# Kernel tuning notes

Measured on AMD Instinct MI355X. Metric: run time of the kernel, lower is better.

Reference implementation:

```python
import jax, jax.numpy as jnp
import numpy as np

B, H, W, DIM = 1, 256, 256, 192
HEADS = 6
K, DIL = 7, 2            # NAttention kernel / dilation
WS, DF = 8, 2            # stripe window size, anchor down factor
AWS = WS // DF           # anchor window size (4)
N1, N2 = WS * WS, AWS * AWS
L = H * W
CPB_HID = 512


def _nbr(size, k, d):
    # 1D neighborhood-attention neighbor indices with dilation (edge-clamped)
    i = np.arange(size); g = i % d; p = i // d
    gsize = size // d  # d divides size
    start = np.clip(p - k // 2, 0, gsize - k)
    nbr_p = start[:, None] + np.arange(k)[None, :]
    nbr = g[:, None] + d * nbr_p                    # absolute key index
    rb = nbr_p - p[:, None] + (k - 1)               # rpb index in [0, 2k-2]
    return nbr.astype(np.int32), rb.astype(np.int32)

NBR_H, RB_H = _nbr(H, K, DIL)
NBR_W, RB_W = _nbr(W, K, DIL)


def _na_attention(q, k, v, rpb):
    # q,k,v: (B, heads, H, W, hd); rpb: (heads, 2K-1, 2K-1)
    bias = rpb[:, RB_H, :]                          # (heads,H,K,2K-1)
    bias = jnp.take(bias, RB_W, axis=3)             # (heads,H,K,W,K)
    bias = jnp.transpose(bias, (0, 1, 3, 2, 4))     # (heads,H,W,K,K)
    logits = []
    for ki in range(K):
        kh = jnp.take(k, NBR_H[:, ki], axis=2)
        for kj in range(K):
            khw = jnp.take(kh, NBR_W[:, kj], axis=3)
            logits.append(jnp.einsum('bnhwc,bnhwc->bnhw', q, khw))
    a = jnp.stack(logits, axis=-1).reshape(*q.shape[:4], K, K) + bias[None]
    a = jax.nn.softmax(a.reshape(*q.shape[:4], K * K), axis=-1).reshape(*q.shape[:4], K, K)
    out = jnp.zeros_like(q)
    for ki in range(K):
        vh = jnp.take(v, NBR_H[:, ki], axis=2)
        for kj in range(K):
            vhw = jnp.take(vh, NBR_W[:, kj], axis=3)
            out = out + a[..., ki, kj, None] * vhw
    return out

na_attention = jax.checkpoint(_na_attention)


def window_partition(x, ws):
    b, h, w, c = x.shape
    x = x.reshape(b, h // ws, ws, w // ws, ws, c)
    return jnp.transpose(x, (0, 1, 3, 2, 4, 5)).reshape(-1, ws * ws, c)


def window_reverse(x, ws, h, w):
    c = x.shape[-1]
    b = x.shape[0] // ((h // ws) * (w // ws))
    x = x.reshape(b, h // ws, w // ws, ws, ws, c)
    return jnp.transpose(x, (0, 1, 3, 2, 4, 5)).reshape(b, h, w, c)


def _l2n(x):
    n = jnp.linalg.norm(x, axis=-1, keepdims=True)
    return x / jnp.maximum(n, 1e-12)


def _affine(attn, table, index, ls, w1, b1, w2):
    # attn: (Bw, heads, Na, Nb)
    attn = attn * jnp.exp(jnp.minimum(ls, float(np.log(100.0))))[None]
    bt = jax.nn.relu(table.reshape(-1, 2) @ w1 + b1) @ w2           # (T, heads)
    bias = bt[index.reshape(-1)].reshape(index.shape[0], index.shape[1], HEADS)
    bias = 16.0 * jax.nn.sigmoid(jnp.transpose(bias, (2, 0, 1)))    # (heads,Na,Nb)
    return attn + bias[None]


def _cos_attn(q, k, v, table, index, ls, w1, b1, w2):
    attn = jnp.einsum('bhnc,bhmc->bhnm', _l2n(q), _l2n(k))
    attn = jax.nn.softmax(_affine(attn, table, index, ls, w1, b1, w2), axis=-1)
    return attn @ v


def _forward(x, h_size, w_size, table, index_a2w, index_w2a, qkv_w, qkv_b,
             anchor_dw_w, anchor_dw_b, anchor_pw_w, anchor_pw_b,
             na_qkv_w, na_qkv_b, na_after_w, na_after_b, na_rpb,
             ls1, cpb1_w1, cpb1_b1, cpb1_w2, ls2, cpb2_w1, cpb2_b1, cpb2_w2,
             proj_w, proj_b):
    Bx, Lx, C = x.shape
    Hs, Ws_ = int(h_size), int(w_size)
    qkv = x @ qkv_w + qkv_b                     # (B,L,3C)
    half = C * 3 // 2
    qkv_window, qkv_stripe = qkv[..., :half], qkv[..., half:]
    # anchor projection: depthwise conv (k=DF+1, stride=DF) + pointwise
    xi = x.reshape(Bx, Hs, Ws_, C)
    a = jax.lax.conv_general_dilated(
        xi, anchor_dw_w, (DF, DF), ((1, 1), (1, 1)),
        dimension_numbers=('NHWC', 'HWIO', 'NHWC'), feature_group_count=C) + anchor_dw_b
    a = a @ anchor_pw_w + anchor_pw_b           # (B, H/DF, W/DF, C//2)
    # ---- neighborhood attention branch ----
    hd = C // HEADS
    xw = qkv_window.reshape(Bx, Hs, Ws_, half)
    q2 = (xw @ na_qkv_w + na_qkv_b).reshape(Bx, Hs, Ws_, 3, HEADS, hd)
    q2 = jnp.transpose(q2, (3, 0, 4, 1, 2, 5))  # (3,B,heads,H,W,hd)
    qn, kn, vn = q2[0] * hd ** -0.5, q2[1], q2[2]
    xna = na_attention(qn, kn, vn, na_rpb)
    xna = jnp.transpose(xna, (0, 2, 3, 1, 4)).reshape(Bx, Hs, Ws_, C)
    xna = (xna @ na_after_w + na_after_b).reshape(Bx, Lx, C // 2)
    # ---- anchor stripe attention branch ----
    qs = window_partition(qkv_stripe.reshape(Bx, Hs, Ws_, half), WS)  # (Bw,N1,1.5C)
    an = window_partition(a, AWS)                                     # (Bw,N2,C//2)
    Bw = qs.shape[0]
    hs = C // 2 // HEADS
    q3 = jnp.transpose(qs.reshape(Bw, N1, 3, HEADS, hs), (2, 0, 3, 1, 4))
    q_s, k_s, v_s = q3[0], q3[1], q3[2]
    an = jnp.transpose(an.reshape(Bw, N2, HEADS, hs), (0, 2, 1, 3))
    x1 = _cos_attn(an, k_s, v_s, table, index_a2w, ls1, cpb1_w1, cpb1_b1, cpb1_w2)
    x2 = _cos_attn(q_s, an, x1, table, index_w2a, ls2, cpb2_w1, cpb2_b1, cpb2_w2)
    x2 = jnp.transpose(x2, (0, 2, 1, 3)).reshape(Bw, N1, C // 2)
    xs = window_reverse(x2, WS, Hs, Ws_).reshape(Bx, Lx, C // 2)
    return jnp.concatenate([xna, xs], axis=-1) @ proj_w + proj_b


def setup_inputs() -> dict:
    key = jax.random.key(0)
    ks = jax.random.split(key, 16)
    f = lambda i, shp, s=0.02: jax.random.normal(ks[i], shp, dtype=jnp.float32) * s
    x = jax.random.normal(ks[0], (B, L, DIM), dtype=jnp.float32)
    # swin-v2 style normalized log-spaced relative coords table
    rc = np.arange(-(WS - 1), WS, dtype=np.float32) / (WS - 1)
    t = np.stack(np.meshgrid(rc, rc, indexing='ij'), axis=-1)[None]
    table = jnp.asarray(np.sign(t) * np.log2(1 + np.abs(t) * 8) / 3.0, dtype=jnp.float32)
    wc = np.arange(WS); ac = np.arange(AWS) * DF
    cw = np.stack(np.meshgrid(wc, wc, indexing='ij'), -1).reshape(-1, 2)
    ca = np.stack(np.meshgrid(ac, ac, indexing='ij'), -1).reshape(-1, 2)
    def _idx(c1, c2):
        d = c1[:, None, :] - c2[None, :, :]
        return jnp.asarray((d[..., 0] + WS - 1) * (2 * WS - 1) + (d[..., 1] + WS - 1), dtype=jnp.int32)
    return {
        'x': x, 'h_size': H, 'w_size': W, 'table': table,
        'index_a2w': _idx(ca, cw), 'index_w2a': _idx(cw, ca),
        'qkv_w': f(1, (DIM, 3 * DIM)), 'qkv_b': jnp.zeros((3 * DIM,), jnp.float32),
        'anchor_dw_w': f(2, (DF + 1, DF + 1, 1, DIM), 0.1),
        'anchor_dw_b': jnp.zeros((DIM,), jnp.float32),
        'anchor_pw_w': f(3, (DIM, DIM // 2)), 'anchor_pw_b': jnp.zeros((DIM // 2,), jnp.float32),
        'na_qkv_w': f(4, (3 * DIM // 2, 3 * DIM)), 'na_qkv_b': jnp.zeros((3 * DIM,), jnp.float32),
        'na_after_w': f(5, (DIM, DIM // 2)), 'na_after_b': jnp.zeros((DIM // 2,), jnp.float32),
        'na_rpb': f(6, (HEADS, 2 * K - 1, 2 * K - 1)),
        'ls1': jnp.log(10.0) * jnp.ones((HEADS, 1, 1), jnp.float32),
        'cpb1_w1': f(7, (2, CPB_HID), 0.1), 'cpb1_b1': jnp.zeros((CPB_HID,), jnp.float32),
        'cpb1_w2': f(8, (CPB_HID, HEADS), 0.1),
        'ls2': jnp.log(10.0) * jnp.ones((HEADS, 1, 1), jnp.float32),
        'cpb2_w1': f(9, (2, CPB_HID), 0.1), 'cpb2_b1': jnp.zeros((CPB_HID,), jnp.float32),
        'cpb2_w2': f(10, (CPB_HID, HEADS), 0.1),
        'proj_w': f(11, (DIM, DIM)), 'proj_b': jnp.zeros((DIM,), jnp.float32),
    }


def reference(x, h_size, w_size, table, index_a2w, index_w2a, qkv_w, qkv_b,
              anchor_dw_w, anchor_dw_b, anchor_pw_w, anchor_pw_b,
              na_qkv_w, na_qkv_b, na_after_w, na_after_b, na_rpb,
              ls1, cpb1_w1, cpb1_b1, cpb1_w2, ls2, cpb2_w1, cpb2_b1, cpb2_w2,
              proj_w, proj_b):
    return _forward(x, h_size, w_size, table, index_a2w, index_w2a, qkv_w, qkv_b,
                    anchor_dw_w, anchor_dw_b, anchor_pw_w, anchor_pw_b,
                    na_qkv_w, na_qkv_b, na_after_w, na_after_b, na_rpb,
                    ls1, cpb1_w1, cpb1_b1, cpb1_w2, ls2, cpb2_w1, cpb2_b1, cpb2_w2,
                    proj_w, proj_b)
```

## Files before the change

kernel.cpp:

```cpp
#include <hip/hip_runtime.h>
#include <math.h>


typedef unsigned short bf16_t;
typedef __attribute__((ext_vector_type(8))) short short8;
typedef __attribute__((ext_vector_type(4))) float f32x4;

__device__ inline float bf2f(bf16_t v) { return __uint_as_float((unsigned)v << 16); }
__device__ inline bf16_t f2bf(float f) {
    unsigned u = __float_as_uint(f);
    unsigned r = (u + 0x7fffu + ((u >> 16) & 1u)) >> 16;
    return (bf16_t)r;
}
__device__ inline float cvt(float v) { return v; }
__device__ inline float cvt(bf16_t v) { return bf2f(v); }
__device__ inline void sto(float* p, float v) { *p = v; }
__device__ inline void sto(bf16_t* p, float v) { *p = f2bf(v); }

__device__ inline void ld_bf8(const bf16_t* p, float* d) {
    uint4 r = *(const uint4*)p;
    d[0] = __uint_as_float(r.x << 16); d[1] = __uint_as_float(r.x & 0xffff0000u);
    d[2] = __uint_as_float(r.y << 16); d[3] = __uint_as_float(r.y & 0xffff0000u);
    d[4] = __uint_as_float(r.z << 16); d[5] = __uint_as_float(r.z & 0xffff0000u);
    d[6] = __uint_as_float(r.w << 16); d[7] = __uint_as_float(r.w & 0xffff0000u);
}
__device__ inline unsigned pk2(float a, float b) {
    return (unsigned)f2bf(a) | ((unsigned)f2bf(b) << 16);
}

template <int KD, int NA, typename TO>
__global__ __launch_bounds__(256) void mfma_gemm_k(
    const bf16_t* __restrict__ A, const bf16_t* __restrict__ Bt,
    const float* __restrict__ bias, TO* __restrict__ C,
    int lda, int ldb, int ldc)
{
    const int t = threadIdx.x;
    const int lane = t & 63, wave = t >> 6;
    const int wr = wave >> 1, wc = wave & 1;
    const int m0 = blockIdx.y * 128 + wr * 64;
    const int n0 = blockIdx.x * 96 + wc * 48;
    const int lm = lane & 15;
    const int q  = lane >> 4;

    f32x4 acc[4][3] = {};
    const bf16_t* ap = A + (size_t)(m0 + lm) * lda + q * 8;
    const bf16_t* bp = Bt + (size_t)(n0 + lm) * ldb + q * 8;

#pragma unroll
    for (int k0 = 0; k0 < KD; k0 += 32) {
        short8 af[4], bf[3];
#pragma unroll
        for (int mi = 0; mi < 4; mi++)
            af[mi] = *(const short8*)(ap + (size_t)(mi * 16) * lda + k0);
#pragma unroll
        for (int ni = 0; ni < 3; ni++)
            bf[ni] = *(const short8*)(bp + (size_t)(ni * 16) * ldb + k0);
#pragma unroll
        for (int mi = 0; mi < 4; mi++)
#pragma unroll
            for (int ni = 0; ni < 3; ni++)
                acc[mi][ni] = __builtin_amdgcn_mfma_f32_16x16x32_bf16(
                    af[mi], bf[ni], acc[mi][ni], 0, 0, 0);
    }

#pragma unroll
    for (int mi = 0; mi < 4; mi++) {
#pragma unroll
        for (int ni = 0; ni < 3; ni++) {
            int col = n0 + ni * 16 + lm;
            float bv = bias[col];
            if (NA) {
                int which = col / 192;
                int hh = (col % 192) / 32;
                int d  = col % 32;
                size_t pbase = ((size_t)which * 6 + hh) * ((size_t)65536 * 32) + d;
#pragma unroll
                for (int r = 0; r < 4; r++) {
                    int row = m0 + mi * 16 + q * 4 + r;
                    int ii = row >> 8, jj = row & 255;
                    int par = ((ii & 1) << 1) | (jj & 1);
                    int pix = par * 16384 + (ii >> 1) * 128 + (jj >> 1);
                    sto(&C[pbase + (size_t)pix * 32], acc[mi][ni][r] + bv);
                }
            } else {
#pragma unroll
                for (int r = 0; r < 4; r++) {
                    int row = m0 + mi * 16 + q * 4 + r;
                    sto(&C[(size_t)row * ldc + col], acc[mi][ni][r] + bv);
                }
            }
        }
    }
}

__global__ __launch_bounds__(256) void cvt_bf16_k(
    const float* __restrict__ src, bf16_t* __restrict__ dst, int n8)
{
    int tid = blockIdx.x * 256 + threadIdx.x;
    if (tid >= n8) return;
    float4 a = ((const float4*)src)[tid * 2];
    float4 b = ((const float4*)src)[tid * 2 + 1];
    uint4 o;
    o.x = pk2(a.x, a.y); o.y = pk2(a.z, a.w);
    o.z = pk2(b.x, b.y); o.w = pk2(b.z, b.w);
    ((uint4*)dst)[tid] = o;
}

__global__ __launch_bounds__(256) void tcvt_k(
    const float* __restrict__ W, bf16_t* __restrict__ Wt,
    int Kd, int N, int ld, int coloff)
{
    int tid = blockIdx.x * 256 + threadIdx.x;
    if (tid >= Kd * N) return;
    int k = tid % Kd, n = tid / Kd;
    Wt[tid] = f2bf(W[(size_t)k * ld + coloff + n]);
}

__global__ __launch_bounds__(256) void tpose_qkvw_k(
    const float* __restrict__ W, float* __restrict__ WT)
{
    int tid = blockIdx.x * 256 + threadIdx.x;
    if (tid >= 288 * 192) return;
    int k = tid % 192, j = tid / 192;
    WT[tid] = W[(size_t)k * 576 + j];
}

__global__ __launch_bounds__(256) void fold_wna_t_k(
    const float* __restrict__ qkv_wT, const float* __restrict__ na_qkv_w,
    bf16_t* __restrict__ Wna_t)
{
    int tid = blockIdx.x * 256 + threadIdx.x;
    if (tid >= 576 * 192) return;
    int k = tid % 192, n = tid / 192;
    float acc = 0.f;
    for (int j = 0; j < 288; j++)
        acc += qkv_wT[j * 192 + k] * na_qkv_w[j * 576 + n];
    Wna_t[tid] = f2bf(acc);
}

__global__ __launch_bounds__(256) void fold_bna_k(
    const float* __restrict__ qkv_b, const float* __restrict__ na_qkv_w,
    const float* __restrict__ na_qkv_b, float* __restrict__ bna)
{
    int j = blockIdx.x * 256 + threadIdx.x;
    if (j >= 576) return;
    float acc = na_qkv_b[j];
    for (int k = 0; k < 288; k++)
        acc += qkv_b[k] * na_qkv_w[k * 576 + j];
    bna[j] = acc;
}

__global__ __launch_bounds__(256) void cpb_k(
    const float* __restrict__ table, const float* __restrict__ w1,
    const float* __restrict__ b1, const float* __restrict__ w2,
    float* __restrict__ bt)
{
    int tid = blockIdx.x * 256 + threadIdx.x;
    if (tid >= 225 * 6) return;
    int h = tid % 6, t = tid / 6;
    float t0 = table[t * 2], t1 = table[t * 2 + 1];
    float acc = 0.f;
    for (int m = 0; m < 512; m++) {
        float hv = t0 * w1[m] + t1 * w1[512 + m] + b1[m];
        hv = fmaxf(hv, 0.f);
        acc += hv * w2[m * 6 + h];
    }
    bt[tid] = acc;
}

#define BM 64
#define BN 64
#define BKK 16
template <typename TA, typename TO>
__global__ __launch_bounds__(256) void gemm_k(
    const TA* __restrict__ A, const float* __restrict__ B,
    const float* __restrict__ bias, TO* __restrict__ C,
    int M, int N, int Kd, int lda, int ldb, int ldc)
{
    __shared__ float As[BKK][BM + 1];
    __shared__ float Bs[BKK][BN + 1];
    const int t  = threadIdx.x;
    const int tx = t & 15, ty = t >> 4;
    const int m0 = blockIdx.y * BM, n0 = blockIdx.x * BN;
    float acc[4][4] = {};

    for (int k0 = 0; k0 < Kd; k0 += BKK) {
#pragma unroll
        for (int i = 0; i < 4; i++) {
            int m = (t >> 4) + i * 16;
            int k = t & 15;
            int gm = m0 + m, gk = k0 + k;
            As[k][m] = (gm < M && gk < Kd) ? cvt(A[(size_t)gm * lda + gk]) : 0.f;
        }
#pragma unroll
        for (int i = 0; i < 4; i++) {
            int k = (t >> 6) + i * 4;
            int n = t & 63;
            int gk = k0 + k, gn = n0 + n;
            Bs[k][n] = (gk < Kd && gn < N) ? B[(size_t)gk * ldb + gn] : 0.f;
        }
        __syncthreads();
#pragma unroll
        for (int k = 0; k < BKK; k++) {
            float a[4], b[4];
#pragma unroll
            for (int i = 0; i < 4; i++) a[i] = As[k][ty * 4 + i];
#pragma unroll
            for (int j = 0; j < 4; j++) b[j] = Bs[k][tx * 4 + j];
#pragma unroll
            for (int i = 0; i < 4; i++)
#pragma unroll
                for (int j = 0; j < 4; j++) acc[i][j] += a[i] * b[j];
        }
        __syncthreads();
    }
#pragma unroll
    for (int i = 0; i < 4; i++) {
        int gm = m0 + ty * 4 + i;
        if (gm >= M) continue;
#pragma unroll
        for (int j = 0; j < 4; j++) {
            int gn = n0 + tx * 4 + j;
            if (gn >= N) continue;
            sto(&C[(size_t)gm * ldc + gn], acc[i][j] + bias[gn]);
        }
    }
}

__global__ __launch_bounds__(256) void dwconv_k(
    const float* __restrict__ x, const float* __restrict__ w,
    const float* __restrict__ b, float* __restrict__ adw)
{
    int tid = blockIdx.x * 256 + threadIdx.x;
    if (tid >= 16384 * 48) return;
    int c4 = tid % 48;
    int p = tid / 48;
    int ow = p & 127, oh = p >> 7;
    int c = c4 * 4;
    float4 s = *(const float4*)(b + c);
#pragma unroll
    for (int kh = 0; kh < 3; kh++) {
        int ih = oh * 2 - 1 + kh;
        if (ih < 0 || ih >= 256) continue;
#pragma unroll
        for (int kw = 0; kw < 3; kw++) {
            int iw = ow * 2 - 1 + kw;
            if (iw < 0 || iw >= 256) continue;
            float4 xv = *(const float4*)(x + (size_t)(ih * 256 + iw) * 192 + c);
            float4 wv = *(const float4*)(w + (kh * 3 + kw) * 192 + c);
            s.x += xv.x * wv.x; s.y += xv.y * wv.y;
            s.z += xv.z * wv.z; s.w += xv.w * wv.w;
        }
    }
    *(float4*)(adw + (size_t)p * 192 + c) = s;
}

__global__ __launch_bounds__(256) void na_attn_k(
    const bf16_t* __restrict__ nap, const float* __restrict__ rpb,
    bf16_t* __restrict__ outp)
{
    __shared__ float rpb_s[176];
    __shared__ __align__(16) unsigned P_s[4][16][20];

    const int t = threadIdx.x;
    const int wv = t >> 6, lane = t & 63;
    const int lm = lane & 15, lq = lane >> 4;
    const int z = blockIdx.z;
    const int h = z >> 2, par = z & 3;

    if (t < 169) rpb_s[t] = rpb[h * 169 + t];
    __syncthreads();

    const int pi  = blockIdx.y;
    const int pj0 = blockIdx.x * 64 + wv * 16;
    const int si  = min(max(pi - 3, 0), 121);
    const int rbh0 = si - pi + 6;
    const int c0  = min(max(pj0 - 3, 0), 121) & ~7;

    const size_t plane = (size_t)65536 * 32;
    const size_t poff  = (size_t)(par * 16384) * 32;
    const bf16_t* qpl = nap + (size_t)h * plane + poff;
    const bf16_t* kpl = nap + (size_t)(6 + h) * plane + poff;
    const bf16_t* vpl = nap + (size_t)(12 + h) * plane + poff;

    const short8 qf = *(const short8*)(qpl + ((size_t)(pi * 128 + pj0 + lm)) * 32 + lq * 8);

    int offc[4][2]; bool vm[4][2];
#pragma unroll
    for (int r = 0; r < 4; r++) {
        int q = lq * 4 + r, pj = pj0 + q;
        int sj = min(max(pj - 3, 0), 121);
#pragma unroll
        for (int t2 = 0; t2 < 2; t2++) {
            int c = c0 + 2 * lm + t2;
            vm[r][t2] = (c >= sj) && (c <= sj + 6);
            offc[r][t2] = min(max(c - pj + 6, 0), 12);
        }
    }
    const int kc0 = min(c0 + 2 * lm,     127) * 64;
    const int kc1 = min(c0 + 2 * lm + 1, 127) * 64;
    int vcoff[8];
#pragma unroll
    for (int i = 0; i < 8; i++) vcoff[i] = min(c0 + lq * 8 + i, 127) * 64;

    const float scale = 0.17677669529663687f;
    f32x4 o0 = {}, o1 = {};
    float sums[4] = {0.f, 0.f, 0.f, 0.f};
    const f32x4 zz = {};

#pragma unroll 2
    for (int rr = 0; rr < 7; rr++) {
        const size_t rb2 = (size_t)((si + rr) * 128) * 64;
        const char* krow = (const char*)kpl + rb2;
        const char* vrow = (const char*)vpl + rb2;

        short8 kf0 = *(const short8*)(krow + kc0 + lq * 16);
        short8 kf1 = *(const short8*)(krow + kc1 + lq * 16);
        f32x4 s0 = __builtin_amdgcn_mfma_f32_16x16x32_bf16(qf, kf0, zz, 0, 0, 0);
        f32x4 s1 = __builtin_amdgcn_mfma_f32_16x16x32_bf16(qf, kf1, zz, 0, 0, 0);

        const float* br = rpb_s + (rbh0 + rr) * 13;
        float e0[4], e1[4];
#pragma unroll
        for (int r = 0; r < 4; r++) {
            float a0 = __expf(fmaf(s0[r], scale, br[offc[r][0]]));
            float a1 = __expf(fmaf(s1[r], scale, br[offc[r][1]]));
            a0 = vm[r][0] ? a0 : 0.f;
            a1 = vm[r][1] ? a1 : 0.f;
            e0[r] = a0; e1[r] = a1;
            sums[r] += a0 + a1;
        }
#pragma unroll
        for (int r = 0; r < 4; r++) {
            unsigned pr;
            asm("v_cvt_pk_bf16_f32 %0, %1, %2" : "=v"(pr) : "v"(e0[r]), "v"(e1[r]));
            P_s[wv][lq * 4 + r][lm] = pr;
        }
        const short8 pf = *(const short8*)((const bf16_t*)P_s[wv][lm] + lq * 8);

        short8 vf0, vf1;
        const char* v0b = vrow + lm * 2;
        const char* v1b = vrow + 32 + lm * 2;
#pragma unroll
        for (int i = 0; i < 8; i++) {
            ((bf16_t*)&vf0)[i] = *(const bf16_t*)(v0b + vcoff[i]);
            ((bf16_t*)&vf1)[i] = *(const bf16_t*)(v1b + vcoff[i]);
        }
        o0 = __builtin_amdgcn_mfma_f32_16x16x32_bf16(pf, vf0, o0, 0, 0, 0);
        o1 = __builtin_amdgcn_mfma_f32_16x16x32_bf16(pf, vf1, o1, 0, 0, 0);
    }

#pragma unroll
    for (int r = 0; r < 4; r++) {
        float s = sums[r];
        s += __shfl_xor(s, 1, 64);
        s += __shfl_xor(s, 2, 64);
        s += __shfl_xor(s, 4, 64);
        s += __shfl_xor(s, 8, 64);
        sums[r] = 1.0f / s;
    }

    const int gi = par >> 1, gj = par & 1;
    const int i0 = pi * 2 + gi;
    bf16_t* ob = outp + ((size_t)i0 * 256 + gj) * 192 + h * 32 + lm;
#pragma unroll
    for (int r = 0; r < 4; r++) {
        int q = lq * 4 + r;
        size_t px = (size_t)(pj0 + q) * 2 * 192;
        ob[px]      = f2bf(o0[r] * sums[r]);
        ob[px + 16] = f2bf(o1[r] * sums[r]);
    }
}

__global__ __launch_bounds__(256) void attn1_k(
    const float* __restrict__ apw,
    const bf16_t* __restrict__ qkvs,
    const float* __restrict__ bt1, const int* __restrict__ idx,
    const float* __restrict__ ls1,
    float* __restrict__ x1)
{
    int tid = blockIdx.x * 256 + threadIdx.x;
    if (tid >= 1024 * 6 * 16) return;
    int n2 = tid & 15;
    int h = (tid >> 4) % 6;
    int w = tid / 96;
    int wi = w >> 5, wj = w & 31;
    float scale = __expf(fminf(ls1[h], 4.605170185988091f));

    int ay = wi * 4 + (n2 >> 2), ax = wj * 4 + (n2 & 3);
    const float* ap = apw + (size_t)(ay * 128 + ax) * 96 + h * 16;
    float qv[16]; float nrm = 0.f;
#pragma unroll
    for (int d = 0; d < 16; d += 4) {
        float4 v = *(const float4*)(ap + d);
        qv[d] = v.x; qv[d + 1] = v.y; qv[d + 2] = v.z; qv[d + 3] = v.w;
        nrm += v.x * v.x + v.y * v.y + v.z * v.z + v.w * v.w;
    }
    float innorm = 1.0f / fmaxf(sqrtf(nrm), 1e-12f);
#pragma unroll
    for (int d = 0; d < 16; d++) qv[d] *= innorm;

    float sum = 0.f;
    float acc[16] = {};
#pragma unroll 4
    for (int m = 0; m < 64; m++) {
        int ky = wi * 8 + (m >> 3), kx = wj * 8 + (m & 7);
        const bf16_t* kp = qkvs + (size_t)(ky * 256 + kx) * 288 + 96 + h * 16;
        float kv[16];
        ld_bf8(kp, kv); ld_bf8(kp + 8, kv + 8);
        float dot = 0.f, kn = 0.f;
#pragma unroll
        for (int d = 0; d < 16; d++) { dot += qv[d] * kv[d]; kn += kv[d] * kv[d]; }
        dot *= 1.0f / fmaxf(sqrtf(kn), 1e-12f);
        float bias = 16.0f / (1.0f + __expf(-bt1[idx[n2 * 64 + m] * 6 + h]));
        float e = __expf(dot * scale + bias);
        sum += e;
        const bf16_t* vp = qkvs + (size_t)(ky * 256 + kx) * 288 + 192 + h * 16;
        float vv[16];
        ld_bf8(vp, vv); ld_bf8(vp + 8, vv + 8);
#pragma unroll
        for (int d = 0; d < 16; d++) acc[d] += e * vv[d];
    }
    float inv = 1.0f / sum;
    float* xp = x1 + ((size_t)w * 6 + h) * 256 + n2 * 16;
#pragma unroll
    for (int d = 0; d < 16; d += 4)
        *(float4*)(xp + d) = make_float4(acc[d] * inv, acc[d + 1] * inv,
                                         acc[d + 2] * inv, acc[d + 3] * inv);
}

__global__ __launch_bounds__(256) void attn2_k(
    const float* __restrict__ apw,
    const bf16_t* __restrict__ qkvs,
    const float* __restrict__ bt2, const int* __restrict__ idx,
    const float* __restrict__ ls2,
    const float* __restrict__ x1,
    bf16_t* __restrict__ cat)
{
    int tid = blockIdx.x * 256 + threadIdx.x;
    if (tid >= 1024 * 6 * 64) return;
    int n1 = tid & 63;
    int h = (tid >> 6) % 6;
    int w = tid / 384;
    int wi = w >> 5, wj = w & 31;
    float scale = __expf(fminf(ls2[h], 4.605170185988091f));

    int qy = wi * 8 + (n1 >> 3), qx = wj * 8 + (n1 & 7);
    const bf16_t* qp = qkvs + (size_t)(qy * 256 + qx) * 288 + h * 16;
    float qv[16];
    ld_bf8(qp, qv); ld_bf8(qp + 8, qv + 8);
    float nrm = 0.f;
#pragma unroll
    for (int d = 0; d < 16; d++) nrm += qv[d] * qv[d];
    float innorm = 1.0f / fmaxf(sqrtf(nrm), 1e-12f);
#pragma unroll
    for (int d = 0; d < 16; d++) qv[d] *= innorm;

    float sum = 0.f;
    float acc[16] = {};
#pragma unroll
    for (int m = 0; m < 16; m++) {
        int ay = wi * 4 + (m >> 2), ax = wj * 4 + (m & 3);
        const float* ap = apw + (size_t)(ay * 128 + ax) * 96 + h * 16;
        float dot = 0.f, kn = 0.f;
#pragma unroll
        for (int d = 0; d < 16; d += 4) {
            float4 v = *(const float4*)(ap + d);
            dot += qv[d] * v.x + qv[d + 1] * v.y + qv[d + 2] * v.z + qv[d + 3] * v.w;
            kn += v.x * v.x + v.y * v.y + v.z * v.z + v.w * v.w;
        }
        dot *= 1.0f / fmaxf(sqrtf(kn), 1e-12f);
        float bias = 16.0f / (1.0f + __expf(-bt2[idx[n1 * 16 + m] * 6 + h]));
        float e = __expf(dot * scale + bias);
        sum += e;
        const float* vp = x1 + ((size_t)w * 6 + h) * 256 + m * 16;
#pragma unroll
        for (int d = 0; d < 16; d += 4) {
            float4 v = *(const float4*)(vp + d);
            acc[d] += e * v.x; acc[d + 1] += e * v.y;
            acc[d + 2] += e * v.z; acc[d + 3] += e * v.w;
        }
    }
    float inv = 1.0f / sum;
#pragma unroll
    for (int d = 0; d < 16; d++) acc[d] *= inv;
    bf16_t* op = cat + (size_t)(qy * 256 + qx) * 192 + 96 + h * 16;
    uint4 o0, o1;
    o0.x = pk2(acc[0], acc[1]);   o0.y = pk2(acc[2], acc[3]);
    o0.z = pk2(acc[4], acc[5]);   o0.w = pk2(acc[6], acc[7]);
    o1.x = pk2(acc[8], acc[9]);   o1.y = pk2(acc[10], acc[11]);
    o1.z = pk2(acc[12], acc[13]); o1.w = pk2(acc[14], acc[15]);
    *(uint4*)(op) = o0;
    *(uint4*)(op + 8) = o1;
}

extern "C" void kernel_launch(void* const* d_in, const int* in_sizes, int n_in,
                              void* d_out, int out_size, void* d_ws, size_t ws_size,
                              hipStream_t stream) {
    const float* x          = (const float*)d_in[0];
    const float* table      = (const float*)d_in[3];
    const int*   idx_a2w    = (const int*)d_in[4];
    const int*   idx_w2a    = (const int*)d_in[5];
    const float* qkv_w      = (const float*)d_in[6];
    const float* qkv_b      = (const float*)d_in[7];
    const float* adw_w      = (const float*)d_in[8];
    const float* adw_b      = (const float*)d_in[9];
    const float* apw_w      = (const float*)d_in[10];
    const float* apw_b      = (const float*)d_in[11];
    const float* na_qkv_w   = (const float*)d_in[12];
    const float* na_qkv_b   = (const float*)d_in[13];
    const float* na_after_w = (const float*)d_in[14];
    const float* na_after_b = (const float*)d_in[15];
    const float* na_rpb     = (const float*)d_in[16];
    const float* ls1        = (const float*)d_in[17];
    const float* cpb1_w1    = (const float*)d_in[18];
    const float* cpb1_b1    = (const float*)d_in[19];
    const float* cpb1_w2    = (const float*)d_in[20];
    const float* ls2        = (const float*)d_in[21];
    const float* cpb2_w1    = (const float*)d_in[22];
    const float* cpb2_b1    = (const float*)d_in[23];
    const float* cpb2_w2    = (const float*)d_in[24];
    const float* proj_w     = (const float*)d_in[25];
    const float* proj_b     = (const float*)d_in[26];
    float* out = (float*)d_out;
    (void)in_sizes; (void)n_in; (void)out_size; (void)ws_size;

    char* base = (char*)d_ws;
    size_t off = 0;
    auto alloc = [&](size_t bytes) {
        off = (off + 255) & ~(size_t)255;
        void* p = base + off; off += bytes; return p;
    };
    float*  bna    = (float*)alloc(576 * 4);
    float*  bt1    = (float*)alloc(225 * 6 * 4);
    float*  bt2    = (float*)alloc(225 * 6 * 4);
    float*  qkv_wT = (float*)alloc(288 * 192 * 4);
    bf16_t* Wna_t  = (bf16_t*)alloc(576 * 192 * 2);
    bf16_t* Ws_t   = (bf16_t*)alloc(288 * 192 * 2);
    bf16_t* Waft_t = (bf16_t*)alloc(96 * 192 * 2);
    bf16_t* Wproj_t= (bf16_t*)alloc(192 * 192 * 2);
    bf16_t* qkvs   = (bf16_t*)alloc((size_t)65536 * 288 * 2);
    char*   naR    = (char*)alloc((size_t)65536 * 576 * 2);
    char*   R      = (char*)alloc((size_t)65536 * 192 * 2);
    float*  apw    = (float*)alloc((size_t)16384 * 96 * 4);
    bf16_t* naqkv   = (bf16_t*)naR;
    float*  x1      = (float*)naR;
    bf16_t* cat     = (bf16_t*)(naR + (8 << 20));
    bf16_t* xb      = (bf16_t*)R;
    float*  adw     = (float*)R;
    bf16_t* xna_pre = (bf16_t*)R;

    tpose_qkvw_k<<<216, 256, 0, stream>>>(qkv_w, qkv_wT);
    fold_wna_t_k<<<432, 256, 0, stream>>>(qkv_wT, na_qkv_w, Wna_t);
    fold_bna_k<<<3, 256, 0, stream>>>(qkv_b, na_qkv_w, na_qkv_b, bna);
    cpb_k<<<6, 256, 0, stream>>>(table, cpb1_w1, cpb1_b1, cpb1_w2, bt1);
    cpb_k<<<6, 256, 0, stream>>>(table, cpb2_w1, cpb2_b1, cpb2_w2, bt2);
    tcvt_k<<<216, 256, 0, stream>>>(qkv_w, Ws_t, 192, 288, 576, 288);
    tcvt_k<<<72, 256, 0, stream>>>(na_after_w, Waft_t, 192, 96, 96, 0);
    tcvt_k<<<144, 256, 0, stream>>>(proj_w, Wproj_t, 192, 192, 192, 0);
    cvt_bf16_k<<<6144, 256, 0, stream>>>(x, xb, 65536 * 192 / 8);

    mfma_gemm_k<192, 0, bf16_t><<<dim3(3, 512), 256, 0, stream>>>(
        xb, Ws_t, qkv_b + 288, qkvs, 192, 192, 288);

    mfma_gemm_k<192, 1, bf16_t><<<dim3(6, 512), 256, 0, stream>>>(
        xb, Wna_t, bna, naqkv, 192, 192, 576);

    dwconv_k<<<3072, 256, 0, stream>>>(x, adw_w, adw_b, adw);
    gemm_k<float, float><<<dim3(2, 256), 256, 0, stream>>>(
        adw, apw_w, apw_b, apw, 16384, 96, 192, 192, 96, 96);

    na_attn_k<<<dim3(2, 128, 24), 256, 0, stream>>>(naqkv, na_rpb, xna_pre);

    mfma_gemm_k<192, 0, bf16_t><<<dim3(1, 512), 256, 0, stream>>>(
        xna_pre, Waft_t, na_after_b, cat, 192, 192, 192);

    attn1_k<<<384, 256, 0, stream>>>(apw, qkvs, bt1, idx_a2w, ls1, x1);
    attn2_k<<<1536, 256, 0, stream>>>(apw, qkvs, bt2, idx_w2a, ls2, x1, cat);

    mfma_gemm_k<192, 0, float><<<dim3(2, 512), 256, 0, stream>>>(
        cat, Wproj_t, proj_b, out, 192, 192, 192);
}
```

Before: 672.4 us.

## Split attn1 key loop across 8 lanes and precompute sigmoid bias tables

attn1 previously ran one thread per (window, head, anchor query) looping over 64 keys with only 384 blocks. Now eight lanes each handle one key row of eight keys, combined with xor-shuffle reductions, which raises the launch to 3072 blocks for more parallelism and latency hiding. Both attention kernels also read a precomputed per-head sigmoid bias table built by a new small kernel, removing the index gather and exp from their inner loops. The cost is shuffle reduction overhead and two extra tiny launches.

```diff
diff --git a/kernel.cpp b/kernel.cpp
--- a/kernel.cpp
+++ b/kernel.cpp
@@ -168,6 +168,16 @@
     bt[tid] = acc;
 }
 
+__global__ __launch_bounds__(256) void sigb_k(
+    const float* __restrict__ bt, const int* __restrict__ idx,
+    float* __restrict__ bp)
+{
+    int tid = blockIdx.x * 256 + threadIdx.x;
+    if (tid >= 6144) return;
+    int h = tid >> 10, p = tid & 1023;
+    bp[tid] = 16.0f / (1.0f + __expf(-bt[idx[p] * 6 + h]));
+}
+
 #define BM 64
 #define BN 64
 #define BKK 16
@@ -375,15 +385,15 @@
 __global__ __launch_bounds__(256) void attn1_k(
     const float* __restrict__ apw,
     const bf16_t* __restrict__ qkvs,
-    const float* __restrict__ bt1, const int* __restrict__ idx,
+    const float* __restrict__ b1p,
     const float* __restrict__ ls1,
     float* __restrict__ x1)
 {
     int tid = blockIdx.x * 256 + threadIdx.x;
-    if (tid >= 1024 * 6 * 16) return;
-    int n2 = tid & 15;
-    int h = (tid >> 4) % 6;
-    int w = tid / 96;
+    int s  = tid & 7;
+    int n2 = (tid >> 3) & 15;
+    int h  = (tid >> 7) % 6;
+    int w  = tid / 768;
     int wi = w >> 5, wj = w & 31;
     float scale = __expf(fminf(ls1[h], 4.605170185988091f));
 
@@ -400,39 +410,49 @@
 #pragma unroll
     for (int d = 0; d < 16; d++) qv[d] *= innorm;
 
+    const float* bp = b1p + h * 1024 + n2 * 64 + s * 8;
+    int ky = wi * 8 + s;
+    const bf16_t* kbase = qkvs + (size_t)(ky * 256 + wj * 8) * 288 + 96 + h * 16;
+
     float sum = 0.f;
     float acc[16] = {};
-#pragma unroll 4
-    for (int m = 0; m < 64; m++) {
-        int ky = wi * 8 + (m >> 3), kx = wj * 8 + (m & 7);
-        const bf16_t* kp = qkvs + (size_t)(ky * 256 + kx) * 288 + 96 + h * 16;
+#pragma unroll
+    for (int j = 0; j < 8; j++) {
+        const bf16_t* kp = kbase + j * 288;
         float kv[16];
         ld_bf8(kp, kv); ld_bf8(kp + 8, kv + 8);
         float dot = 0.f, kn = 0.f;
 #pragma unroll
         for (int d = 0; d < 16; d++) { dot += qv[d] * kv[d]; kn += kv[d] * kv[d]; }
         dot *= 1.0f / fmaxf(sqrtf(kn), 1e-12f);
-        float bias = 16.0f / (1.0f + __expf(-bt1[idx[n2 * 64 + m] * 6 + h]));
-        float e = __expf(dot * scale + bias);
+        float e = __expf(fmaf(dot, scale, bp[j]));
         sum += e;
-        const bf16_t* vp = qkvs + (size_t)(ky * 256 + kx) * 288 + 192 + h * 16;
+        const bf16_t* vp = kp + 96;
         float vv[16];
         ld_bf8(vp, vv); ld_bf8(vp + 8, vv + 8);
 #pragma unroll
         for (int d = 0; d < 16; d++) acc[d] += e * vv[d];
     }
-    float inv = 1.0f / sum;
-    float* xp = x1 + ((size_t)w * 6 + h) * 256 + n2 * 16;
-#pragma unroll
-    for (int d = 0; d < 16; d += 4)
-        *(float4*)(xp + d) = make_float4(acc[d] * inv, acc[d + 1] * inv,
-                                         acc[d + 2] * inv, acc[d + 3] * inv);
+#pragma unroll
+    for (int msk = 1; msk < 8; msk <<= 1) {
+        sum += __shfl_xor(sum, msk, 64);
+#pragma unroll
+        for (int d = 0; d < 16; d++) acc[d] += __shfl_xor(acc[d], msk, 64);
+    }
+    if (s == 0) {
+        float inv = 1.0f / sum;
+        float* xp = x1 + ((size_t)w * 6 + h) * 256 + n2 * 16;
+#pragma unroll
+        for (int d = 0; d < 16; d += 4)
+            *(float4*)(xp + d) = make_float4(acc[d] * inv, acc[d + 1] * inv,
+                                             acc[d + 2] * inv, acc[d + 3] * inv);
+    }
 }
 
 __global__ __launch_bounds__(256) void attn2_k(
     const float* __restrict__ apw,
     const bf16_t* __restrict__ qkvs,
-    const float* __restrict__ bt2, const int* __restrict__ idx,
+    const float* __restrict__ b2p,
     const float* __restrict__ ls2,
     const float* __restrict__ x1,
     bf16_t* __restrict__ cat)
@@ -456,6 +476,7 @@
 #pragma unroll
     for (int d = 0; d < 16; d++) qv[d] *= innorm;
 
+    const float* bp = b2p + h * 1024 + n1 * 16;
     float sum = 0.f;
     float acc[16] = {};
 #pragma unroll
@@ -470,8 +491,7 @@
             kn += v.x * v.x + v.y * v.y + v.z * v.z + v.w * v.w;
         }
         dot *= 1.0f / fmaxf(sqrtf(kn), 1e-12f);
-        float bias = 16.0f / (1.0f + __expf(-bt2[idx[n1 * 16 + m] * 6 + h]));
-        float e = __expf(dot * scale + bias);
+        float e = __expf(fmaf(dot, scale, bp[m]));
         sum += e;
         const float* vp = x1 + ((size_t)w * 6 + h) * 256 + m * 16;
 #pragma unroll
@@ -534,6 +554,8 @@
     float*  bna    = (float*)alloc(576 * 4);
     float*  bt1    = (float*)alloc(225 * 6 * 4);
     float*  bt2    = (float*)alloc(225 * 6 * 4);
+    float*  b1p    = (float*)alloc(6144 * 4);
+    float*  b2p    = (float*)alloc(6144 * 4);
     float*  qkv_wT = (float*)alloc(288 * 192 * 4);
     bf16_t* Wna_t  = (bf16_t*)alloc(576 * 192 * 2);
     bf16_t* Ws_t   = (bf16_t*)alloc(288 * 192 * 2);
@@ -555,6 +577,8 @@
     fold_bna_k<<<3, 256, 0, stream>>>(qkv_b, na_qkv_w, na_qkv_b, bna);
     cpb_k<<<6, 256, 0, stream>>>(table, cpb1_w1, cpb1_b1, cpb1_w2, bt1);
     cpb_k<<<6, 256, 0, stream>>>(table, cpb2_w1, cpb2_b1, cpb2_w2, bt2);
+    sigb_k<<<24, 256, 0, stream>>>(bt1, idx_a2w, b1p);
+    sigb_k<<<24, 256, 0, stream>>>(bt2, idx_w2a, b2p);
     tcvt_k<<<216, 256, 0, stream>>>(qkv_w, Ws_t, 192, 288, 576, 288);
     tcvt_k<<<72, 256, 0, stream>>>(na_after_w, Waft_t, 192, 96, 96, 0);
     tcvt_k<<<144, 256, 0, stream>>>(proj_w, Wproj_t, 192, 192, 192, 0);
@@ -575,8 +599,8 @@
     mfma_gemm_k<192, 0, bf16_t><<<dim3(1, 512), 256, 0, stream>>>(
         xna_pre, Waft_t, na_after_b, cat, 192, 192, 192);
 
-    attn1_k<<<384, 256, 0, stream>>>(apw, qkvs, bt1, idx_a2w, ls1, x1);
-    attn2_k<<<1536, 256, 0, stream>>>(apw, qkvs, bt2, idx_w2a, ls2, x1, cat);
+    attn1_k<<<3072, 256, 0, stream>>>(apw, qkvs, b1p, ls1, x1);
+    attn2_k<<<1536, 256, 0, stream>>>(apw, qkvs, b2p, ls2, x1, cat);
 
     mfma_gemm_k<192, 0, float><<<dim3(2, 512), 256, 0, stream>>>(
         cat, Wproj_t, proj_b, out, 192, 192, 192);
```

Result: no change. 666.5 us (-0.9%).
